# Kernel tuning notes

Hardware: AMD Instinct MI355X
Metric: run time of the kernel (lower is better)

The kernel has to match this reference:

```python
import jax, jax.numpy as jnp
import numpy as np

NUM_GRAPHS = 128

def _gcn_conv(x, W, b, src, dst, deg_inv_sqrt, n_nodes):
    # PyG GCNConv: h = X W; out[dst] += d^-1/2[src] * d^-1/2[dst] * h[src]; out += b
    h = x @ W
    norm = deg_inv_sqrt[src] * deg_inv_sqrt[dst]  # [E]
    msg = h[src] * norm[:, None]                  # [E, C]
    out = jax.ops.segment_sum(msg, dst, num_segments=n_nodes)
    return out + b


def setup_inputs() -> dict:
    key = jax.random.key(0)
    k1, k2, k3, k4, k5 = jax.random.split(key, 5)
    n_nodes, n_edges, c_in, c_hid = 50000, 800000, 256, 256
    x = jax.random.normal(k1, (n_nodes, c_in), dtype=jnp.float32)
    edge_index = jax.random.randint(k2, (2, n_edges), 0, n_nodes, dtype=jnp.int64)
    batch = jnp.sort(jax.random.randint(k3, (n_nodes,), 0, NUM_GRAPHS, dtype=jnp.int64))
    s1 = 1.0 / np.sqrt(c_in)
    s2 = 1.0 / np.sqrt(c_hid)
    W1 = jax.random.uniform(k4, (c_in, c_hid), jnp.float32, -s1, s1)
    b1 = jnp.zeros((c_hid,), jnp.float32)
    W2 = jax.random.uniform(k5, (c_hid, c_hid), jnp.float32, -s2, s2)
    b2 = jnp.zeros((c_hid,), jnp.float32)
    return {"x": x, "edge_index": edge_index, "batch": batch,
            "W1": W1, "b1": b1, "W2": W2, "b2": b2}


def reference(x, edge_index, batch, W1, b1, W2, b2):
    n_nodes = x.shape[0]
    # add self-loops (GCNConv default add_self_loops=True)
    loops = jnp.arange(n_nodes, dtype=edge_index.dtype)
    src = jnp.concatenate([edge_index[0], loops])
    dst = jnp.concatenate([edge_index[1], loops])
    deg = jax.ops.segment_sum(jnp.ones_like(dst, dtype=x.dtype), dst, num_segments=n_nodes)
    deg_inv_sqrt = jnp.where(deg > 0, jax.lax.rsqrt(deg), 0.0)

    h = jax.nn.relu(_gcn_conv(x, W1, b1, src, dst, deg_inv_sqrt, n_nodes))
    # dropout p=0.2 is identity in eval mode
    h = jax.nn.relu(_gcn_conv(h, W2, b2, src, dst, deg_inv_sqrt, n_nodes))

    # global mean pool over graph ids
    sums = jax.ops.segment_sum(h, batch, num_segments=NUM_GRAPHS)
    cnts = jax.ops.segment_sum(jnp.ones((n_nodes,), h.dtype), batch, num_segments=NUM_GRAPHS)
    return sums / jnp.maximum(cnts, 1.0)[:, None]
```

## Files before the change

### kernel.cpp

```cpp
#include <hip/hip_runtime.h>

#define NCH 256
#define NS  16

typedef short short8 __attribute__((ext_vector_type(8)));
typedef float f32x4  __attribute__((ext_vector_type(4)));

__device__ __forceinline__ float b2f(unsigned short u) {
    union { unsigned int i; float f; } x; x.i = ((unsigned int)u) << 16; return x.f;
}
__device__ __forceinline__ unsigned short f2b(float f) {
    unsigned int u = __float_as_uint(f);
    unsigned int r = (u + 0x7FFFu + ((u >> 16) & 1u)) >> 16;
    return (unsigned short)r;
}

#define GLOAD_LDS16(gptr, lptr) \
    __builtin_amdgcn_global_load_lds((const __attribute__((address_space(1))) void*)(gptr), \
                                     (__attribute__((address_space(3))) void*)(lptr), 16, 0, 0)

__global__ __launch_bounds__(256) void k_hist(const int* __restrict__ dst, int E,
                                              int* __restrict__ deg) {
    int e = blockIdx.x * 256 + threadIdx.x;
    if (e < E) atomicAdd(&deg[dst[e]], 1);
}

__global__ __launch_bounds__(256) void k_scan_blk(const int* __restrict__ deg,
                                                  int* __restrict__ part,
                                                  int* __restrict__ bsum, int N) {
    __shared__ int sm[256];
    int t = threadIdx.x;
    int base = blockIdx.x * 1024 + t * 4;
    int v[4]; int s = 0;
#pragma unroll
    for (int j = 0; j < 4; ++j) {
        int i = base + j;
        int d = (i < N) ? deg[i] : 0;
        v[j] = d; s += d;
    }
    sm[t] = s; __syncthreads();
#pragma unroll
    for (int off = 1; off < 256; off <<= 1) {
        int u = (t >= off) ? sm[t - off] : 0;
        __syncthreads();
        sm[t] += u;
        __syncthreads();
    }
    int excl = sm[t] - s;
#pragma unroll
    for (int j = 0; j < 4; ++j) {
        int i = base + j;
        if (i < N) part[i] = excl;
        excl += v[j];
    }
    if (t == 255) bsum[blockIdx.x] = sm[255];
}

__global__ void k_scan_top(int* __restrict__ bsum, int nb, int* __restrict__ rowptr_end) {
    int t = threadIdx.x;
    int orig = (t < nb) ? bsum[t] : 0;
    int v = orig;
#pragma unroll
    for (int off = 1; off < 64; off <<= 1) {
        int u = __shfl_up(v, off, 64);
        if (t >= off) v += u;
    }
    if (t < nb) bsum[t] = v - orig;
    if (t == 63) *rowptr_end = v;
}

__global__ __launch_bounds__(256) void k_finalize(const int* __restrict__ deg,
                                                  int* __restrict__ row_ptr,
                                                  const int* __restrict__ boff,
                                                  int* __restrict__ cursor,
                                                  float* __restrict__ dinv, int N) {
    int i = blockIdx.x * 256 + threadIdx.x;
    if (i < N) {
        int rp = row_ptr[i] + boff[i >> 10];
        row_ptr[i] = rp;
        cursor[i]  = rp;
        dinv[i] = rsqrtf((float)(deg[i] + 1));
    }
}

__global__ __launch_bounds__(256) void k_scatter_sh(const int* __restrict__ src,
                                                    const int* __restrict__ dst, int E,
                                                    int* __restrict__ cursor,
                                                    const float* __restrict__ dinv,
                                                    int2* __restrict__ cw,
                                                    unsigned shmul) {
    const int shard  = blockIdx.x & 7;
    const int nchunk = gridDim.x >> 3;
    const int chunk  = blockIdx.x >> 3;
    const int per = (E + nchunk - 1) / nchunk;
    const int e0 = chunk * per;
    const int e1 = min(e0 + per, E);
    for (int e = e0 + threadIdx.x; e < e1; e += 256) {
        int d = dst[e];
        int s = (int)__umulhi((unsigned)d, shmul);
        if (s == shard) {
            int sv = src[e];
            int pos = atomicAdd(&cursor[d], 1);
            cw[pos] = make_int2(sv, __float_as_int(dinv[sv]));
        }
    }
}

__global__ __launch_bounds__(256) void k_cast8(const float* __restrict__ in,
                                               unsigned short* __restrict__ out, int n8) {
    int i = blockIdx.x * 256 + threadIdx.x;
    if (i < n8) {
        const float4* p = (const float4*)(in + (size_t)i * 8);
        float4 a = p[0], b = p[1];
        unsigned short us[8];
        us[0] = f2b(a.x); us[1] = f2b(a.y); us[2] = f2b(a.z); us[3] = f2b(a.w);
        us[4] = f2b(b.x); us[5] = f2b(b.y); us[6] = f2b(b.z); us[7] = f2b(b.w);
        *(int4*)(out + (size_t)i * 8) = *(const int4*)us;
    }
}

__global__ __launch_bounds__(256) void k_castT(const float* __restrict__ W1,
                                               const float* __restrict__ W2,
                                               unsigned short* __restrict__ Wt1,
                                               unsigned short* __restrict__ Wt2) {
    int k = blockIdx.x, n = threadIdx.x;
    const float* W = blockIdx.y ? W2 : W1;
    unsigned short* Wt = blockIdx.y ? Wt2 : Wt1;
    Wt[(size_t)n * 256 + k] = f2b(W[(size_t)k * 256 + n]);
}

__global__ __launch_bounds__(512, 4) void k_gemm_lds(const unsigned short* __restrict__ A,
                                                     const unsigned short* __restrict__ Bt,
                                                     unsigned short* __restrict__ C,
                                                     int M, int tiles) {
    __shared__ unsigned short As[32 * 256];

    const int tid  = threadIdx.x;
    const int w    = tid >> 6;
    const int lane = tid & 63;
    const int lr   = lane & 15;
    const int ku   = lane >> 4;

    short8 bfr[2][8];
    {
        const unsigned short* pb = Bt + (size_t)(w * 32 + lr) * NCH + ku * 8;
#pragma unroll
        for (int nf = 0; nf < 2; ++nf)
#pragma unroll
            for (int ks = 0; ks < 8; ++ks)
                bfr[nf][ks] = *(const short8*)(pb + nf * 16 * NCH + ks * 32);
    }

    const int gu0 = w * 128 + lane;
    for (int t = blockIdx.x; t < tiles; t += gridDim.x) {
        __syncthreads();
#pragma unroll
        for (int j = 0; j < 2; ++j) {
            int gu = gu0 + j * 64;
            int r  = gu >> 5;
            int u  = gu & 31;
            int grow = t * 32 + r; if (grow >= M) grow = M - 1;
            const unsigned short* gp = A + (size_t)grow * NCH + ((u ^ (r & 7)) << 3);
            GLOAD_LDS16(gp, As + (size_t)(w * 128 + j * 64) * 8);
        }
        __syncthreads();

        f32x4 acc[2][2];
#pragma unroll
        for (int rf = 0; rf < 2; ++rf)
#pragma unroll
            for (int nf = 0; nf < 2; ++nf) acc[rf][nf] = (f32x4){0.f, 0.f, 0.f, 0.f};

#pragma unroll
        for (int ks = 0; ks < 8; ++ks) {
#pragma unroll
            for (int rf = 0; rf < 2; ++rf) {
                int row = rf * 16 + lr;
                int uu  = (ks * 4 + ku) ^ (row & 7);
                short8 af = *(const short8*)&As[row * 256 + uu * 8];
                acc[rf][0] = __builtin_amdgcn_mfma_f32_16x16x32_bf16(bfr[0][ks], af,
                                                                     acc[rf][0], 0, 0, 0);
                acc[rf][1] = __builtin_amdgcn_mfma_f32_16x16x32_bf16(bfr[1][ks], af,
                                                                     acc[rf][1], 0, 0, 0);
            }
        }

#pragma unroll
        for (int rf = 0; rf < 2; ++rf) {
            int row = t * 32 + rf * 16 + lr;
            if (row < M) {
                unsigned short* pc = C + (size_t)row * NCH + w * 32 + ku * 4;
#pragma unroll
                for (int nf = 0; nf < 2; ++nf) {
                    unsigned short us[4];
                    us[0] = f2b(acc[rf][nf][0]); us[1] = f2b(acc[rf][nf][1]);
                    us[2] = f2b(acc[rf][nf][2]); us[3] = f2b(acc[rf][nf][3]);
                    *(int2*)(pc + nf * 16) = *(const int2*)us;
                }
            }
        }
    }
}

__global__ __launch_bounds__(256) void k_agg_w(const unsigned short* __restrict__ h,
                                               const float* __restrict__ dinv,
                                               const int* __restrict__ row_ptr,
                                               const int2* __restrict__ cw,
                                               const float* __restrict__ bias,
                                               unsigned short* __restrict__ out, int M) {
    int v = blockIdx.x * 4 + (threadIdx.x >> 6);
    if (v >= M) return;
    const int lane = threadIdx.x & 63;
    const int half = lane >> 5;
    const int cb   = (lane & 31) << 3;

    float acc[8] = {};
    float dv = dinv[v];

    short8 rs = {};
    if (half == 0) rs = *(const short8*)&h[(size_t)v * NCH + cb];

    int beg = row_ptr[v], end = row_ptr[v + 1];
    int i0 = beg + half * 2;

    short8 r0 = {}, r1 = {};
    float  w0 = 0.f, w1 = 0.f;
    bool b0 = i0 < end, b1 = i0 + 1 < end;
    if (b0) {
        int2 e = cw[i0];
        r0 = *(const short8*)&h[(size_t)e.x * NCH + cb];
        w0 = __int_as_float(e.y);
    }
    if (b1) {
        int2 e = cw[i0 + 1];
        r1 = *(const short8*)&h[(size_t)e.x * NCH + cb];
        w1 = __int_as_float(e.y);
    }

    while (b0) {
        int in = i0 + 4;
        bool n0 = in < end, n1 = in + 1 < end;
        short8 s0 = {}, s1 = {};
        float  x0 = 0.f, x1 = 0.f;
        if (n0) {
            int2 e = cw[in];
            s0 = *(const short8*)&h[(size_t)e.x * NCH + cb];
            x0 = __int_as_float(e.y);
        }
        if (n1) {
            int2 e = cw[in + 1];
            s1 = *(const short8*)&h[(size_t)e.x * NCH + cb];
            x1 = __int_as_float(e.y);
        }
#pragma unroll
        for (int i = 0; i < 8; ++i) acc[i] += w0 * b2f((unsigned short)r0[i]);
#pragma unroll
        for (int i = 0; i < 8; ++i) acc[i] += w1 * b2f((unsigned short)r1[i]);
        r0 = s0; r1 = s1; w0 = x0; w1 = x1; b0 = n0; b1 = n1; i0 = in;
    }

    if (half == 0) {
#pragma unroll
        for (int i = 0; i < 8; ++i) acc[i] += dv * b2f((unsigned short)rs[i]);
    }

#pragma unroll
    for (int i = 0; i < 8; ++i) acc[i] += __shfl_xor(acc[i], 32, 64);

    if (half == 0) {
        f32x4 bl = *(const f32x4*)&bias[cb];
        f32x4 bh = *(const f32x4*)&bias[cb + 4];
        unsigned short us[8];
#pragma unroll
        for (int i = 0; i < 8; ++i) {
            float b = (i < 4) ? bl[i] : bh[i - 4];
            us[i] = f2b(fmaxf(dv * acc[i] + b, 0.0f));
        }
        *(int4*)&out[(size_t)v * NCH + cb] = *(const int4*)us;
    }
}

__device__ __forceinline__ int lower_bound_i(const int* a, int n, int key) {
    int lo = 0, hi = n;
    while (lo < hi) {
        int mid = (lo + hi) >> 1;
        if (a[mid] < key) lo = mid + 1; else hi = mid;
    }
    return lo;
}

__global__ __launch_bounds__(64) void k_pool_a(const unsigned short* __restrict__ a,
                                               const int* __restrict__ batch,
                                               float* __restrict__ partial, int N) {
    int g = blockIdx.x, s = blockIdx.y;
    const int lane = threadIdx.x;
    const int half = lane >> 5;
    const int cb   = (lane & 31) << 3;

    int lo = lower_bound_i(batch, N, g);
    int hi = lower_bound_i(batch, N, g + 1);
    int cnt = hi - lo;
    int len = (cnt + NS - 1) / NS;
    int rlo = lo + s * len;
    int rhi = min(rlo + len, hi);

    float acc[8] = {};
    for (int r = rlo + half; r < rhi; r += 2) {
        short8 hv = *(const short8*)&a[(size_t)r * NCH + cb];
#pragma unroll
        for (int i = 0; i < 8; ++i) acc[i] += b2f((unsigned short)hv[i]);
    }
#pragma unroll
    for (int i = 0; i < 8; ++i) acc[i] += __shfl_xor(acc[i], 32, 64);

    if (half == 0) {
        float* p = partial + ((size_t)g * NS + s) * NCH + cb;
        *(f32x4*)p       = (f32x4){acc[0], acc[1], acc[2], acc[3]};
        *(f32x4*)(p + 4) = (f32x4){acc[4], acc[5], acc[6], acc[7]};
    }
}

__global__ __launch_bounds__(256) void k_pool_b(const float* __restrict__ partial,
                                                const int* __restrict__ batch,
                                                float* __restrict__ out, int N) {
    int g = blockIdx.x, ch = threadIdx.x;
    int lo = lower_bound_i(batch, N, g);
    int hi = lower_bound_i(batch, N, g + 1);
    float s = 0.0f;
#pragma unroll
    for (int k = 0; k < NS; ++k)
        s += partial[((size_t)g * NS + k) * NCH + ch];
    out[(size_t)g * NCH + ch] = s / (float)max(hi - lo, 1);
}

extern "C" void kernel_launch(void* const* d_in, const int* in_sizes, int n_in,
                              void* d_out, int out_size, void* d_ws, size_t ws_size,
                              hipStream_t stream) {
    const float* x     = (const float*)d_in[0];
    const int*   ei    = (const int*)d_in[1];
    const int*   batch = (const int*)d_in[2];
    const float* W1    = (const float*)d_in[3];
    const float* b1    = (const float*)d_in[4];
    const float* W2    = (const float*)d_in[5];
    const float* b2    = (const float*)d_in[6];
    float* out = (float*)d_out;

    const int M = in_sizes[0] / NCH;
    const int E = in_sizes[1] / 2;
    const int* src = ei;
    const int* dst = ei + E;

    char* w = (char*)d_ws;
    auto alloc = [&](size_t bytes) -> void* {
        void* p = (void*)w;
        w += (bytes + 255) & ~(size_t)255;
        return p;
    };
    int*   deg     = (int*)alloc((size_t)M * 4);
    float* dinv    = (float*)alloc((size_t)M * 4);
    int*   row_ptr = (int*)alloc((size_t)(M + 1) * 4);
    int*   cursor  = (int*)alloc((size_t)M * 4);
    int*   bsum    = (int*)alloc(64 * 4);
    int2*  cw      = (int2*)alloc((size_t)E * 8);
    unsigned short* xb   = (unsigned short*)alloc((size_t)M * NCH * 2);
    unsigned short* bufP = (unsigned short*)alloc((size_t)M * NCH * 2);
    unsigned short* bufQ = (unsigned short*)alloc((size_t)M * NCH * 2);
    unsigned short* Wt1  = (unsigned short*)alloc((size_t)NCH * NCH * 2);
    unsigned short* Wt2  = (unsigned short*)alloc((size_t)NCH * NCH * 2);
    float* partial = (float*)alloc((size_t)128 * NS * NCH * 4);

    const int nb = (M + 1023) / 1024;
    const unsigned shmul = (unsigned)(((8ull << 32) + M - 1) / (unsigned long long)M);
    const int tiles = (M + 31) / 32;

    k_cast8<<<(M * NCH / 8 + 255) / 256, 256, 0, stream>>>(x, xb, M * NCH / 8);
    k_castT<<<dim3(256, 2), 256, 0, stream>>>(W1, W2, Wt1, Wt2);

    hipMemsetAsync(deg, 0, (size_t)M * 4, stream);
    k_hist<<<(E + 255) / 256, 256, 0, stream>>>(dst, E, deg);
    k_scan_blk<<<nb, 256, 0, stream>>>(deg, row_ptr, bsum, M);
    k_scan_top<<<1, 64, 0, stream>>>(bsum, nb, row_ptr + M);
    k_finalize<<<(M + 255) / 256, 256, 0, stream>>>(deg, row_ptr, bsum, cursor, dinv, M);
    k_scatter_sh<<<2048, 256, 0, stream>>>(src, dst, E, cursor, dinv, cw, shmul);

    const int ggrid = 512;
    const int agrid = (M + 3) / 4;

    k_gemm_lds<<<ggrid, 512, 0, stream>>>(xb, Wt1, bufP, M, tiles);
    k_agg_w<<<agrid, 256, 0, stream>>>(bufP, dinv, row_ptr, cw, b1, bufQ, M);
    k_gemm_lds<<<ggrid, 512, 0, stream>>>(bufQ, Wt2, bufP, M, tiles);
    k_agg_w<<<agrid, 256, 0, stream>>>(bufP, dinv, row_ptr, cw, b2, bufQ, M);
    k_pool_a<<<dim3(128, NS), 64, 0, stream>>>(bufQ, batch, partial, M);
    k_pool_b<<<128, 256, 0, stream>>>(partial, batch, out, M);
}
```

Before: 287.7 us.

## Fuse x bf16 cast into first GEMM and merge histogram with weight transpose

Result: slower. 306.5 us (+6.5%).

```diff
diff --git a/kernel.cpp b/kernel.cpp
--- a/kernel.cpp
+++ b/kernel.cpp
@@ -19,10 +19,33 @@
     __builtin_amdgcn_global_load_lds((const __attribute__((address_space(1))) void*)(gptr), \
                                      (__attribute__((address_space(3))) void*)(lptr), 16, 0, 0)
 
-__global__ __launch_bounds__(256) void k_hist(const int* __restrict__ dst, int E,
-                                              int* __restrict__ deg) {
-    int e = blockIdx.x * 256 + threadIdx.x;
-    if (e < E) atomicAdd(&deg[dst[e]], 1);
+__global__ __launch_bounds__(256) void k_pre(const int* __restrict__ dst, int E,
+                                             int* __restrict__ deg, int nh,
+                                             unsigned shmul,
+                                             const float* __restrict__ W1,
+                                             const float* __restrict__ W2,
+                                             unsigned short* __restrict__ Wt1,
+                                             unsigned short* __restrict__ Wt2) {
+    int b = blockIdx.x;
+    if (b < nh) {
+        const int shard  = b & 7;
+        const int nchunk = nh >> 3;
+        const int chunk  = b >> 3;
+        const int per = (E + nchunk - 1) / nchunk;
+        const int e0 = chunk * per;
+        const int e1 = min(e0 + per, E);
+        for (int e = e0 + threadIdx.x; e < e1; e += 256) {
+            int d = dst[e];
+            if ((int)__umulhi((unsigned)d, shmul) == shard)
+                atomicAdd(&deg[d], 1);
+        }
+    } else {
+        int k = (b - nh) & 255;
+        const float* W = ((b - nh) >> 8) ? W2 : W1;
+        unsigned short* Wt = ((b - nh) >> 8) ? Wt2 : Wt1;
+        int n = threadIdx.x;
+        Wt[(size_t)n * 256 + k] = f2b(W[(size_t)k * 256 + n]);
+    }
 }
 
 __global__ __launch_bounds__(256) void k_scan_blk(const int* __restrict__ deg,
@@ -106,100 +129,116 @@
     }
 }
 
-__global__ __launch_bounds__(256) void k_cast8(const float* __restrict__ in,
-                                               unsigned short* __restrict__ out, int n8) {
-    int i = blockIdx.x * 256 + threadIdx.x;
-    if (i < n8) {
-        const float4* p = (const float4*)(in + (size_t)i * 8);
-        float4 a = p[0], b = p[1];
-        unsigned short us[8];
-        us[0] = f2b(a.x); us[1] = f2b(a.y); us[2] = f2b(a.z); us[3] = f2b(a.w);
-        us[4] = f2b(b.x); us[5] = f2b(b.y); us[6] = f2b(b.z); us[7] = f2b(b.w);
-        *(int4*)(out + (size_t)i * 8) = *(const int4*)us;
-    }
-}
-
-__global__ __launch_bounds__(256) void k_castT(const float* __restrict__ W1,
-                                               const float* __restrict__ W2,
-                                               unsigned short* __restrict__ Wt1,
-                                               unsigned short* __restrict__ Wt2) {
-    int k = blockIdx.x, n = threadIdx.x;
-    const float* W = blockIdx.y ? W2 : W1;
-    unsigned short* Wt = blockIdx.y ? Wt2 : Wt1;
-    Wt[(size_t)n * 256 + k] = f2b(W[(size_t)k * 256 + n]);
-}
-
-__global__ __launch_bounds__(512, 4) void k_gemm_lds(const unsigned short* __restrict__ A,
-                                                     const unsigned short* __restrict__ Bt,
-                                                     unsigned short* __restrict__ C,
-                                                     int M, int tiles) {
+
+__device__ __forceinline__ void gemm_compute_store(const unsigned short* As,
+                                                   const short8 bfr[2][8],
+                                                   unsigned short* __restrict__ C,
+                                                   int M, int t, int w, int lr, int ku) {
+    f32x4 acc[2][2];
+#pragma unroll
+    for (int rf = 0; rf < 2; ++rf)
+#pragma unroll
+        for (int nf = 0; nf < 2; ++nf) acc[rf][nf] = (f32x4){0.f, 0.f, 0.f, 0.f};
+
+#pragma unroll
+    for (int ks = 0; ks < 8; ++ks) {
+#pragma unroll
+        for (int rf = 0; rf < 2; ++rf) {
+            int row = rf * 16 + lr;
+            int uu  = (ks * 4 + ku) ^ (row & 7);
+            short8 af = *(const short8*)&As[row * 256 + uu * 8];
+            acc[rf][0] = __builtin_amdgcn_mfma_f32_16x16x32_bf16(bfr[0][ks], af,
+                                                                 acc[rf][0], 0, 0, 0);
+            acc[rf][1] = __builtin_amdgcn_mfma_f32_16x16x32_bf16(bfr[1][ks], af,
+                                                                 acc[rf][1], 0, 0, 0);
+        }
+    }
+
+#pragma unroll
+    for (int rf = 0; rf < 2; ++rf) {
+        int row = t * 32 + rf * 16 + lr;
+        if (row < M) {
+            unsigned short* pc = C + (size_t)row * NCH + w * 32 + ku * 4;
+#pragma unroll
+            for (int nf = 0; nf < 2; ++nf) {
+                unsigned short us[4];
+                us[0] = f2b(acc[rf][nf][0]); us[1] = f2b(acc[rf][nf][1]);
+                us[2] = f2b(acc[rf][nf][2]); us[3] = f2b(acc[rf][nf][3]);
+                *(int2*)(pc + nf * 16) = *(const int2*)us;
+            }
+        }
+    }
+}
+
+__device__ __forceinline__ void load_bfr(const unsigned short* __restrict__ Bt,
+                                         short8 bfr[2][8], int w, int lr, int ku) {
+    const unsigned short* pb = Bt + (size_t)(w * 32 + lr) * NCH + ku * 8;
+#pragma unroll
+    for (int nf = 0; nf < 2; ++nf)
+#pragma unroll
+        for (int ks = 0; ks < 8; ++ks)
+            bfr[nf][ks] = *(const short8*)(pb + nf * 16 * NCH + ks * 32);
+}
+
+__global__ __launch_bounds__(512, 4) void k_gemm2(const unsigned short* __restrict__ A,
+                                                  const unsigned short* __restrict__ Bt,
+                                                  unsigned short* __restrict__ C, int M) {
     __shared__ unsigned short As[32 * 256];
-
     const int tid  = threadIdx.x;
     const int w    = tid >> 6;
     const int lane = tid & 63;
     const int lr   = lane & 15;
     const int ku   = lane >> 4;
+    const int t    = blockIdx.x;
 
     short8 bfr[2][8];
-    {
-        const unsigned short* pb = Bt + (size_t)(w * 32 + lr) * NCH + ku * 8;
-#pragma unroll
-        for (int nf = 0; nf < 2; ++nf)
-#pragma unroll
-            for (int ks = 0; ks < 8; ++ks)
-                bfr[nf][ks] = *(const short8*)(pb + nf * 16 * NCH + ks * 32);
-    }
-
-    const int gu0 = w * 128 + lane;
-    for (int t = blockIdx.x; t < tiles; t += gridDim.x) {
-        __syncthreads();
-#pragma unroll
-        for (int j = 0; j < 2; ++j) {
-            int gu = gu0 + j * 64;
-            int r  = gu >> 5;
-            int u  = gu & 31;
-            int grow = t * 32 + r; if (grow >= M) grow = M - 1;
-            const unsigned short* gp = A + (size_t)grow * NCH + ((u ^ (r & 7)) << 3);
-            GLOAD_LDS16(gp, As + (size_t)(w * 128 + j * 64) * 8);
-        }
-        __syncthreads();
-
-        f32x4 acc[2][2];
-#pragma unroll
-        for (int rf = 0; rf < 2; ++rf)
-#pragma unroll
-            for (int nf = 0; nf < 2; ++nf) acc[rf][nf] = (f32x4){0.f, 0.f, 0.f, 0.f};
-
-#pragma unroll
-        for (int ks = 0; ks < 8; ++ks) {
-#pragma unroll
-            for (int rf = 0; rf < 2; ++rf) {
-                int row = rf * 16 + lr;
-                int uu  = (ks * 4 + ku) ^ (row & 7);
-                short8 af = *(const short8*)&As[row * 256 + uu * 8];
-                acc[rf][0] = __builtin_amdgcn_mfma_f32_16x16x32_bf16(bfr[0][ks], af,
-                                                                     acc[rf][0], 0, 0, 0);
-                acc[rf][1] = __builtin_amdgcn_mfma_f32_16x16x32_bf16(bfr[1][ks], af,
-                                                                     acc[rf][1], 0, 0, 0);
-            }
-        }
-
-#pragma unroll
-        for (int rf = 0; rf < 2; ++rf) {
-            int row = t * 32 + rf * 16 + lr;
-            if (row < M) {
-                unsigned short* pc = C + (size_t)row * NCH + w * 32 + ku * 4;
-#pragma unroll
-                for (int nf = 0; nf < 2; ++nf) {
-                    unsigned short us[4];
-                    us[0] = f2b(acc[rf][nf][0]); us[1] = f2b(acc[rf][nf][1]);
-                    us[2] = f2b(acc[rf][nf][2]); us[3] = f2b(acc[rf][nf][3]);
-                    *(int2*)(pc + nf * 16) = *(const int2*)us;
-                }
-            }
-        }
-    }
+    load_bfr(Bt, bfr, w, lr, ku);
+
+#pragma unroll
+    for (int j = 0; j < 2; ++j) {
+        int gu = w * 128 + j * 64 + lane;
+        int r  = gu >> 5;
+        int u  = gu & 31;
+        int grow = t * 32 + r; if (grow >= M) grow = M - 1;
+        const unsigned short* gp = A + (size_t)grow * NCH + ((u ^ (r & 7)) << 3);
+        GLOAD_LDS16(gp, As + (size_t)(w * 128 + j * 64) * 8);
+    }
+    __syncthreads();
+
+    gemm_compute_store(As, bfr, C, M, t, w, lr, ku);
+}
+
+__global__ __launch_bounds__(512, 4) void k_gemm1(const float* __restrict__ A,
+                                                  const unsigned short* __restrict__ Bt,
+                                                  unsigned short* __restrict__ C, int M) {
+    __shared__ unsigned short As[32 * 256];
+    const int tid  = threadIdx.x;
+    const int w    = tid >> 6;
+    const int lane = tid & 63;
+    const int lr   = lane & 15;
+    const int ku   = lane >> 4;
+    const int t    = blockIdx.x;
+
+    short8 bfr[2][8];
+    load_bfr(Bt, bfr, w, lr, ku);
+
+#pragma unroll
+    for (int j = 0; j < 2; ++j) {
+        int unit = tid + j * 512;
+        int r = unit >> 5;
+        int u = unit & 31;
+        int grow = t * 32 + r; if (grow >= M) grow = M - 1;
+        const float* pa = A + (size_t)grow * NCH + u * 8;
+        float4 f0 = *(const float4*)pa;
+        float4 f1 = *(const float4*)(pa + 4);
+        unsigned short us[8];
+        us[0] = f2b(f0.x); us[1] = f2b(f0.y); us[2] = f2b(f0.z); us[3] = f2b(f0.w);
+        us[4] = f2b(f1.x); us[5] = f2b(f1.y); us[6] = f2b(f1.z); us[7] = f2b(f1.w);
+        *(int4*)&As[r * 256 + ((u ^ (r & 7)) << 3)] = *(const int4*)us;
+    }
+    __syncthreads();
+
+    gemm_compute_store(As, bfr, C, M, t, w, lr, ku);
 }
 
 __global__ __launch_bounds__(256) void k_agg_w(const unsigned short* __restrict__ h,
@@ -362,7 +401,6 @@
     int*   cursor  = (int*)alloc((size_t)M * 4);
     int*   bsum    = (int*)alloc(64 * 4);
     int2*  cw      = (int2*)alloc((size_t)E * 8);
-    unsigned short* xb   = (unsigned short*)alloc((size_t)M * NCH * 2);
     unsigned short* bufP = (unsigned short*)alloc((size_t)M * NCH * 2);
     unsigned short* bufQ = (unsigned short*)alloc((size_t)M * NCH * 2);
     unsigned short* Wt1  = (unsigned short*)alloc((size_t)NCH * NCH * 2);
@@ -372,23 +410,20 @@
     const int nb = (M + 1023) / 1024;
     const unsigned shmul = (unsigned)(((8ull << 32) + M - 1) / (unsigned long long)M);
     const int tiles = (M + 31) / 32;
-
-    k_cast8<<<(M * NCH / 8 + 255) / 256, 256, 0, stream>>>(x, xb, M * NCH / 8);
-    k_castT<<<dim3(256, 2), 256, 0, stream>>>(W1, W2, Wt1, Wt2);
+    const int nh = 2048;
 
     hipMemsetAsync(deg, 0, (size_t)M * 4, stream);
-    k_hist<<<(E + 255) / 256, 256, 0, stream>>>(dst, E, deg);
+    k_pre<<<nh + 512, 256, 0, stream>>>(dst, E, deg, nh, shmul, W1, W2, Wt1, Wt2);
     k_scan_blk<<<nb, 256, 0, stream>>>(deg, row_ptr, bsum, M);
     k_scan_top<<<1, 64, 0, stream>>>(bsum, nb, row_ptr + M);
     k_finalize<<<(M + 255) / 256, 256, 0, stream>>>(deg, row_ptr, bsum, cursor, dinv, M);
-    k_scatter_sh<<<2048, 256, 0, stream>>>(src, dst, E, cursor, dinv, cw, shmul);
-
-    const int ggrid = 512;
+    k_scatter_sh<<<4096, 256, 0, stream>>>(src, dst, E, cursor, dinv, cw, shmul);
+
     const int agrid = (M + 3) / 4;
 
-    k_gemm_lds<<<ggrid, 512, 0, stream>>>(xb, Wt1, bufP, M, tiles);
+    k_gemm1<<<tiles, 512, 0, stream>>>(x, Wt1, bufP, M);
     k_agg_w<<<agrid, 256, 0, stream>>>(bufP, dinv, row_ptr, cw, b1, bufQ, M);
-    k_gemm_lds<<<ggrid, 512, 0, stream>>>(bufQ, Wt2, bufP, M, tiles);
+    k_gemm2<<<tiles, 512, 0, stream>>>(bufQ, Wt2, bufP, M);
     k_agg_w<<<agrid, 256, 0, stream>>>(bufP, dinv, row_ptr, cw, b2, bufQ, M);
     k_pool_a<<<dim3(128, NS), 64, 0, stream>>>(bufQ, batch, partial, M);
     k_pool_b<<<128, 256, 0, stream>>>(partial, batch, out, M);
```
